# Optimization experiments

Measured on AMD Instinct MI355X. Metric: run time of the kernel, lower is better.

## Reference

```python
import jax, jax.numpy as jnp
import numpy as np

B, T, C = 2, 2048, 2048
H, KV, D = 16, 4, 128   # n_head, n_kv_head, head_dim
EPS = 1.1920929e-07     # torch.finfo(float32).eps, F.rms_norm default


def setup_inputs() -> dict:
    key = jax.random.key(0)
    ks = jax.random.split(key, 7)
    x = jax.random.normal(ks[0], (B, T, C), dtype=jnp.float32)
    # rope angles: cos/sin of positions, broadcastable to [B,T,H,D//2]
    inv_freq = 1.0 / (10000.0 ** (jnp.arange(0, D // 2, dtype=jnp.float32) / (D // 2)))
    ang = jnp.arange(T, dtype=jnp.float32)[:, None] * inv_freq[None, :]
    cos = jnp.cos(ang)[None, :, None, :]  # [1,T,1,D/2]
    sin = jnp.sin(ang)[None, :, None, :]
    s = 0.02
    Wq = jax.random.normal(ks[1], (C, H * D), dtype=jnp.float32) * s
    Wk = jax.random.normal(ks[2], (C, KV * D), dtype=jnp.float32) * s
    Wv = jax.random.normal(ks[3], (C, KV * D), dtype=jnp.float32) * s
    Wo = jax.random.normal(ks[4], (C, C), dtype=jnp.float32) * s
    return {"x": x, "cos": cos, "sin": sin, "Wq": Wq, "Wk": Wk, "Wv": Wv, "Wo": Wo}


def _rope(t, cos, sin):
    d = t.shape[-1] // 2
    t1, t2 = t[..., :d], t[..., d:]
    return jnp.concatenate([t1 * cos + t2 * sin, -t1 * sin + t2 * cos], axis=-1)


def _rmsnorm(t):
    return t * jax.lax.rsqrt(jnp.mean(t * t, axis=-1, keepdims=True) + EPS)


def reference(x, cos, sin, Wq, Wk, Wv, Wo):
    q = (x @ Wq).reshape(B, T, H, D)
    k = (x @ Wk).reshape(B, T, KV, D)
    v = (x @ Wv).reshape(B, T, KV, D)
    q = _rmsnorm(_rope(q, cos, sin))
    k = _rmsnorm(_rope(k, cos, sin))
    # [B, KV, G, T, D] query grouped per kv head (GQA)
    G = H // KV
    qh = q.transpose(0, 2, 1, 3).reshape(B, KV, G, T, D)
    kh = k.transpose(0, 2, 1, 3)  # [B, KV, T, D]
    vh = v.transpose(0, 2, 1, 3)
    scale = 1.0 / np.sqrt(D).astype(np.float32)
    scores = jnp.einsum('bhgqd,bhkd->bhgqk', qh, kh) * scale
    causal = jnp.tril(jnp.ones((T, T), dtype=bool))
    scores = jnp.where(causal, scores, jnp.finfo(scores.dtype).min)
    attn = jax.nn.softmax(scores, axis=-1)
    y = jnp.einsum('bhgqk,bhkd->bhgqd', attn, vh)  # [B,KV,G,T,D]
    y = y.reshape(B, H, T, D).transpose(0, 2, 1, 3).reshape(B, T, C)
    return y @ Wo
```

## Files before the change

### kernel.cpp

```cpp
#include <hip/hip_runtime.h>

using bf16x8 = __attribute__((ext_vector_type(8))) short;
using f32x4  = __attribute__((ext_vector_type(4))) float;

#define B_  2
#define T_  2048
#define C_  2048
#define H_  16
#define KV_ 4
#define D_  128

__device__ __forceinline__ unsigned short f2b(float f) {
  union { float f; unsigned int u; } v; v.f = f;
  unsigned int r = v.u + 0x7fffu + ((v.u >> 16) & 1u);
  return (unsigned short)(r >> 16);
}
__device__ __forceinline__ float b2f(unsigned short u) {
  union { unsigned int u; float f; } v; v.u = ((unsigned int)u) << 16;
  return v.f;
}
__device__ __forceinline__ unsigned int cvt_pk_bf16(float lo, float hi) {
  unsigned int r;
  asm("v_cvt_pk_bf16_f32 %0, %1, %2" : "=v"(r) : "v"(lo), "v"(hi));
  return r;
}
__device__ __forceinline__ void gld_lds16(const void* g, void* l) {
  __builtin_amdgcn_global_load_lds(
      (__attribute__((address_space(1))) void*)g,
      (__attribute__((address_space(3))) void*)l, 16, 0, 0);
}

__global__ void cast_bf16_k(const float* __restrict__ in, unsigned short* __restrict__ out) {
  int i = blockIdx.x * 256 + threadIdx.x;
  float4 f = ((const float4*)in)[i];
  ushort4 u; u.x = f2b(f.x); u.y = f2b(f.y); u.z = f2b(f.z); u.w = f2b(f.w);
  ((ushort4*)out)[i] = u;
}

__global__ void wtrans(const float* __restrict__ W, unsigned short* __restrict__ Wt,
                       int K, int N) {
  __shared__ float s[32][33];
  int n0 = blockIdx.x * 32, k0 = blockIdx.y * 32;
  int tx = threadIdx.x, ty = threadIdx.y;
  #pragma unroll
  for (int yy = 0; yy < 32; yy += 8)
    s[ty + yy][tx] = W[(size_t)(k0 + ty + yy) * N + n0 + tx];
  __syncthreads();
  #pragma unroll
  for (int yy = 0; yy < 32; yy += 8)
    Wt[(size_t)(n0 + ty + yy) * K + k0 + tx] = f2b(s[tx][ty + yy]);
}

template <bool OUT_BF16>
__device__ __forceinline__ void gemm_tile(
    const unsigned short* __restrict__ A, const unsigned short* __restrict__ Bt,
    void* __restrict__ Cv, int K, int ldc, int m0, int n0b, int n0c,
    unsigned short* sA, unsigned short* sB)
{
  const int tid  = threadIdx.x;
  const int lane = tid & 63, w = tid >> 6;
  const int quad = lane >> 4, l16 = lane & 15;
  const int wm = (w >> 1) * 64, wn = (w & 1) * 64;

  f32x4 acc[4][4] = {};

  const unsigned short* Abase = A  + (size_t)m0  * K;
  const unsigned short* Bbase = Bt + (size_t)n0b * K;

  for (int k0 = 0; k0 < K; k0 += 32) {
    #pragma unroll
    for (int r = 0; r < 2; ++r) {
      int c = tid + r * 256;
      int row = c >> 2, col = (c & 3) * 8;
      gld_lds16(Abase + (size_t)row * K + k0 + col, sA + c * 8);
      gld_lds16(Bbase + (size_t)row * K + k0 + col, sB + c * 8);
    }
    __syncthreads();
    bf16x8 af[4], bfr[4];
    #pragma unroll
    for (int i = 0; i < 4; ++i)
      af[i]  = *(const bf16x8*)(sA + (wm + i * 16 + l16) * 32 + quad * 8);
    #pragma unroll
    for (int j = 0; j < 4; ++j)
      bfr[j] = *(const bf16x8*)(sB + (wn + j * 16 + l16) * 32 + quad * 8);
    #pragma unroll
    for (int i = 0; i < 4; ++i)
      #pragma unroll
      for (int j = 0; j < 4; ++j)
        acc[i][j] = __builtin_amdgcn_mfma_f32_16x16x32_bf16(af[i], bfr[j], acc[i][j], 0, 0, 0);
    __syncthreads();
  }
  #pragma unroll
  for (int i = 0; i < 4; ++i) {
    #pragma unroll
    for (int r = 0; r < 4; ++r) {
      int row = m0 + wm + i * 16 + quad * 4 + r;
      #pragma unroll
      for (int j = 0; j < 4; ++j) {
        int col = n0c + wn + j * 16 + l16;
        float v = acc[i][j][r];
        if (OUT_BF16) ((unsigned short*)Cv)[(size_t)row * ldc + col] = f2b(v);
        else          ((float*)Cv)[(size_t)row * ldc + col] = v;
      }
    }
  }
}

__global__ void qkv_gemm(const unsigned short* __restrict__ xb,
                         const unsigned short* __restrict__ Wqt,
                         const unsigned short* __restrict__ Wkt,
                         const unsigned short* __restrict__ Wvt,
                         unsigned short* q, unsigned short* k, unsigned short* v) {
  __shared__ unsigned short sA[128 * 32], sB[128 * 32];
  int nt = blockIdx.x, mt = blockIdx.y;
  const unsigned short* Bt; unsigned short* C; int n0, ldc;
  if (nt < 16)      { Bt = Wqt; C = q; n0 = nt * 128;        ldc = H_ * D_;  }
  else if (nt < 20) { Bt = Wkt; C = k; n0 = (nt - 16) * 128; ldc = KV_ * D_; }
  else              { Bt = Wvt; C = v; n0 = (nt - 20) * 128; ldc = KV_ * D_; }
  gemm_tile<true>(xb, Bt, C, C_, ldc, mt * 128, n0, n0, sA, sB);
}

__global__ void out_gemm(const unsigned short* __restrict__ yb,
                         const unsigned short* __restrict__ Wot,
                         float* __restrict__ out) {
  __shared__ unsigned short sA[128 * 32], sB[128 * 32];
  gemm_tile<false>(yb, Wot, out, C_, C_, blockIdx.y * 128, blockIdx.x * 128, blockIdx.x * 128,
                   sA, sB);
}

template <int NH>
__global__ void ropenorm(const unsigned short* __restrict__ in,
                         const float* __restrict__ cs, const float* __restrict__ sn,
                         unsigned short* __restrict__ out, float oscale) {
  int row  = blockIdx.x * 4 + (threadIdx.x >> 6);
  int lane = threadIdx.x & 63;
  int head = row % NH;
  int t = (row / NH) & (T_ - 1);
  int b = row / (NH * T_);
  const unsigned short* p = in + (size_t)row * D_;
  float t1 = b2f(p[lane]), t2 = b2f(p[lane + 64]);
  float c = cs[t * 64 + lane], s = sn[t * 64 + lane];
  float o1 = t1 * c + t2 * s;
  float o2 = t2 * c - t1 * s;
  float ss = o1 * o1 + o2 * o2;
  #pragma unroll
  for (int off = 32; off > 0; off >>= 1) ss += __shfl_xor(ss, off, 64);
  float r = rsqrtf(ss * (1.0f / 128.0f) + 1.1920929e-07f) * oscale;
  size_t base = ((size_t)((b * NH + head) * 128 + (t >> 4))) * 2048 + (size_t)(t & 15) * 8;
  out[base + (size_t)(lane >> 3) * 128 + (lane & 7)]       = f2b(o1 * r);
  out[base + (size_t)(8 + (lane >> 3)) * 128 + (lane & 7)] = f2b(o2 * r);
}

__global__ void vfrag_k(const unsigned short* __restrict__ v, unsigned short* __restrict__ vf) {
  int it = blockIdx.x;
  int b = blockIdx.y >> 2, kv = blockIdx.y & 3;
  int d = threadIdx.x, ty = threadIdx.y;
  int t0 = it * 64;
  size_t obase = ((size_t)((b * KV_ + kv) * 32 + it)) * 8192
               + (size_t)(d >> 4) * 1024 + (size_t)(d & 15) * 8;
  #pragma unroll
  for (int tcg = 0; tcg < 4; ++tcg) {
    int tc = ty * 4 + tcg;
    unsigned short val[8];
    #pragma unroll
    for (int e = 0; e < 8; ++e)
      val[e] = v[(((size_t)(b * T_) + t0 + tc * 8 + e) * KV_ + kv) * D_ + d];
    ushort4 u0 = {val[0], val[1], val[2], val[3]};
    ushort4 u1 = {val[4], val[5], val[6], val[7]};
    *(ushort4*)(vf + obase + (size_t)tc * 128)     = u0;
    *(ushort4*)(vf + obase + (size_t)tc * 128 + 4) = u1;
  }
}

__global__ __launch_bounds__(256, 2) void attn_kernel(
    const unsigned short* __restrict__ qf, const unsigned short* __restrict__ kf,
    const unsigned short* __restrict__ vf, unsigned short* __restrict__ yb) {
  __shared__ __align__(16) char smem[34048];

  const int xp = (int)blockIdx.x;
  const int b = xp >> 2, kv = xp & 3;
  const int yp = (int)blockIdx.y;
  const int j = yp >> 2, hp = yp & 3;
  const int tid = threadIdx.x;
  const int w = tid >> 6, lane = tid & 63;
  const int quad = lane >> 4, l16 = lane & 15;
  const int qsel = w & 1, half = w >> 1;
  const int qt = qsel ? (63 - j) : j;
  const int h = kv * 4 + hp;
  const int q0 = qt * 32;
  const int ntile = (qt >> 1) + 1;
  unsigned short* myP = (unsigned short*)smem + w * (32 * 72);

  const unsigned short* Qf = qf + ((size_t)(b * H_ + h) * 128 + qt * 2) * 2048;
  const unsigned short* Kf = kf + (size_t)(b * KV_ + kv) * 128 * 2048;
  const unsigned short* Vf = vf + (size_t)(b * KV_ + kv) * 32 * 8192;

  bf16x8 bq[2][4];
  #pragma unroll
  for (int i = 0; i < 2; ++i)
    #pragma unroll
    for (int kk = 0; kk < 4; ++kk)
      bq[i][kk] = *(const bf16x8*)(Qf + (size_t)i * 2048 + (kk * 4 + quad) * 128 + l16 * 8);

  float l_i[2] = {0.f, 0.f};
  f32x4 o[2][8] = {};

  for (int it = half; it < ntile; it += 2) {
    const int t0 = it * 64;
    const unsigned short* Kt = Kf + (size_t)(it * 4) * 2048;
    const unsigned short* Vt = Vf + (size_t)it * 8192;

    f32x4 sc[4][2] = {};
    #pragma unroll
    for (int kk = 0; kk < 4; ++kk) {
      bf16x8 ak[4];
      #pragma unroll
      for (int jt = 0; jt < 4; ++jt)
        ak[jt] = *(const bf16x8*)(Kt + (size_t)jt * 2048 + (kk * 4 + quad) * 128 + l16 * 8);
      #pragma unroll
      for (int jt = 0; jt < 4; ++jt)
        #pragma unroll
        for (int i = 0; i < 2; ++i)
          sc[jt][i] = __builtin_amdgcn_mfma_f32_16x16x32_bf16(ak[jt], bq[i][kk], sc[jt][i], 0, 0, 0);
    }

    bf16x8 bv[2][8];
    #pragma unroll
    for (int kk2 = 0; kk2 < 2; ++kk2)
      #pragma unroll
      for (int jj = 0; jj < 8; ++jj)
        bv[kk2][jj] = *(const bf16x8*)(Vt + (size_t)jj * 1024 + (kk2 * 4 + quad) * 128 + l16 * 8);

    if (it == ntile - 1) {
      #pragma unroll
      for (int jt = 0; jt < 4; ++jt) {
        int kg = t0 + jt * 16 + quad * 4;
        #pragma unroll
        for (int i = 0; i < 2; ++i) {
          int qg = q0 + i * 16 + l16;
          #pragma unroll
          for (int r = 0; r < 4; ++r)
            if (kg + r > qg) sc[jt][i][r] = -3.0e38f;
        }
      }
    }

    #pragma unroll
    for (int i = 0; i < 2; ++i) {
      float part = 0.f;
      #pragma unroll
      for (int jt = 0; jt < 4; ++jt)
        #pragma unroll
        for (int r = 0; r < 4; ++r) {
          float p = __expf(sc[jt][i][r] - 12.0f);
          sc[jt][i][r] = p; part += p;
        }
      l_i[i] += part;
    }

    #pragma unroll
    for (int i = 0; i < 2; ++i)
      #pragma unroll
      for (int jt = 0; jt < 4; ++jt) {
        uint2 uu;
        uu.x = cvt_pk_bf16(sc[jt][i][0], sc[jt][i][1]);
        uu.y = cvt_pk_bf16(sc[jt][i][2], sc[jt][i][3]);
        *(uint2*)(myP + (i * 16 + l16) * 72 + jt * 16 + quad * 4) = uu;
      }

    #pragma unroll
    for (int kk2 = 0; kk2 < 2; ++kk2) {
      bf16x8 ap[2];
      #pragma unroll
      for (int i = 0; i < 2; ++i)
        ap[i] = *(const bf16x8*)(myP + (i * 16 + l16) * 72 + kk2 * 32 + quad * 8);
      #pragma unroll
      for (int i = 0; i < 2; ++i)
        #pragma unroll
        for (int jj = 0; jj < 8; ++jj)
          o[i][jj] = __builtin_amdgcn_mfma_f32_16x16x32_bf16(ap[i], bv[kk2][jj], o[i][jj], 0, 0, 0);
    }
  }

  float lsum[2];
  #pragma unroll
  for (int i = 0; i < 2; ++i) {
    float l = l_i[i];
    l += __shfl_xor(l, 16, 64);
    l += __shfl_xor(l, 32, 64);
    lsum[i] = l;
  }

  __syncthreads();
  float* oc = (float*)smem + qsel * (32 * 132);
  float* lc = (float*)smem + 2 * (32 * 132) + qsel * 32;
  if (half == 1) {
    #pragma unroll
    for (int i = 0; i < 2; ++i) {
      if (quad == 0) lc[i * 16 + l16] = lsum[i];
      #pragma unroll
      for (int jj = 0; jj < 8; ++jj)
        #pragma unroll
        for (int r = 0; r < 4; ++r)
          oc[(i * 16 + quad * 4 + r) * 132 + jj * 16 + l16] = o[i][jj][r];
    }
  }
  __syncthreads();
  if (half == 0) {
    #pragma unroll
    for (int i = 0; i < 2; ++i) {
      float l = lsum[i] + lc[i * 16 + l16];
      float linv = 1.0f / l;
      float lr[4];
      #pragma unroll
      for (int r = 0; r < 4; ++r) lr[r] = __shfl(linv, quad * 4 + r, 64);
      #pragma unroll
      for (int r = 0; r < 4; ++r) {
        int tg = q0 + i * 16 + quad * 4 + r;
        unsigned short* yr = yb + (((size_t)(b * T_ + tg)) * H_ + h) * D_;
        #pragma unroll
        for (int jj = 0; jj < 8; ++jj) {
          float vsum = o[i][jj][r] + oc[(i * 16 + quad * 4 + r) * 132 + jj * 16 + l16];
          yr[jj * 16 + l16] = f2b(vsum * lr[r]);
        }
      }
    }
  }
}

extern "C" void kernel_launch(void* const* d_in, const int* in_sizes, int n_in,
                              void* d_out, int out_size, void* d_ws, size_t ws_size,
                              hipStream_t stream) {
  (void)in_sizes; (void)n_in; (void)out_size; (void)ws_size;
  const float* x  = (const float*)d_in[0];
  const float* cs = (const float*)d_in[1];
  const float* sn = (const float*)d_in[2];
  const float* Wq = (const float*)d_in[3];
  const float* Wk = (const float*)d_in[4];
  const float* Wv = (const float*)d_in[5];
  const float* Wo = (const float*)d_in[6];
  float* out = (float*)d_out;
  char* ws = (char*)d_ws;

  unsigned short* xb   = (unsigned short*)(ws + 0);
  unsigned short* Wqt  = (unsigned short*)(ws + 16777216);
  unsigned short* Wkt  = (unsigned short*)(ws + 25165824);
  unsigned short* Wvt  = (unsigned short*)(ws + 27262976);
  unsigned short* Wot  = (unsigned short*)(ws + 29360128);
  unsigned short* qraw = (unsigned short*)(ws + 37748736);
  unsigned short* kraw = (unsigned short*)(ws + 54525952);
  unsigned short* vraw = (unsigned short*)(ws + 58720256);
  unsigned short* qfr  = (unsigned short*)(ws + 62914560);
  unsigned short* kfr  = (unsigned short*)(ws + 79691776);
  unsigned short* vfr  = (unsigned short*)(ws + 83886080);
  unsigned short* yb   = qraw;

  cast_bf16_k<<<dim3(8192), dim3(256), 0, stream>>>(x, xb);
  wtrans<<<dim3(64, 64), dim3(32, 8), 0, stream>>>(Wq, Wqt, 2048, 2048);
  wtrans<<<dim3(16, 64), dim3(32, 8), 0, stream>>>(Wk, Wkt, 2048, 512);
  wtrans<<<dim3(16, 64), dim3(32, 8), 0, stream>>>(Wv, Wvt, 2048, 512);
  wtrans<<<dim3(64, 64), dim3(32, 8), 0, stream>>>(Wo, Wot, 2048, 2048);
  qkv_gemm<<<dim3(24, 32), dim3(256), 0, stream>>>(xb, Wqt, Wkt, Wvt, qraw, kraw, vraw);
  ropenorm<16><<<dim3(16384), dim3(256), 0, stream>>>(qraw, cs, sn, qfr, 0.08838834764831845f);
  ropenorm<4><<<dim3(4096),  dim3(256), 0, stream>>>(kraw, cs, sn, kfr, 1.0f);
  vfrag_k<<<dim3(32, 8), dim3(128, 2), 0, stream>>>(vraw, vfr);
  attn_kernel<<<dim3(8, 128), dim3(256), 0, stream>>>(qfr, kfr, vfr, yb);
  out_gemm<<<dim3(16, 32), dim3(256), 0, stream>>>(yb, Wot, out);
}
```

Before: 318.5 us.

## Replace QKV GEMM with 256x256 tile, 8-wave, double-buffered direct-to-LDS kernel

Replaces the 128x128 QKV projection GEMM with a 256x256-tile kernel using 512 threads, async global-to-LDS loads into double-buffered swizzled LDS, and interleaved MFMA/load phases with priority hints. Blocks are remapped so each XCD handles adjacent M rows, which improves L2 reuse of the x tile. The goal is higher arithmetic intensity and overlap of memory loads with MFMA work. In exchange, 192 blocks on 256 CUs leaves some CUs idle, and the large LDS and register footprint reduces occupancy.

```diff
diff --git a/kernel.cpp b/kernel.cpp
--- a/kernel.cpp
+++ b/kernel.cpp
@@ -106,26 +106,149 @@
   }
 }
 
-__global__ void qkv_gemm(const unsigned short* __restrict__ xb,
-                         const unsigned short* __restrict__ Wqt,
-                         const unsigned short* __restrict__ Wkt,
-                         const unsigned short* __restrict__ Wvt,
-                         unsigned short* q, unsigned short* k, unsigned short* v) {
-  __shared__ unsigned short sA[128 * 32], sB[128 * 32];
-  int nt = blockIdx.x, mt = blockIdx.y;
-  const unsigned short* Bt; unsigned short* C; int n0, ldc;
-  if (nt < 16)      { Bt = Wqt; C = q; n0 = nt * 128;        ldc = H_ * D_;  }
-  else if (nt < 20) { Bt = Wkt; C = k; n0 = (nt - 16) * 128; ldc = KV_ * D_; }
-  else              { Bt = Wvt; C = v; n0 = (nt - 20) * 128; ldc = KV_ * D_; }
-  gemm_tile<true>(xb, Bt, C, C_, ldc, mt * 128, n0, n0, sA, sB);
-}
-
 __global__ void out_gemm(const unsigned short* __restrict__ yb,
                          const unsigned short* __restrict__ Wot,
                          float* __restrict__ out) {
   __shared__ unsigned short sA[128 * 32], sB[128 * 32];
   gemm_tile<false>(yb, Wot, out, C_, C_, blockIdx.y * 128, blockIdx.x * 128, blockIdx.x * 128,
                    sA, sB);
+}
+
+__global__ __launch_bounds__(512, 2) void qkv_gemm8(
+    const unsigned short* __restrict__ xb,
+    const unsigned short* __restrict__ Wqt,
+    const unsigned short* __restrict__ Wkt,
+    const unsigned short* __restrict__ Wvt,
+    unsigned short* __restrict__ q, unsigned short* __restrict__ k,
+    unsigned short* __restrict__ v) {
+  __shared__ unsigned short lds[65536];
+
+  const int id  = (int)blockIdx.x;
+  const int xcd = id & 7, jj = id >> 3;
+  const int mt  = xcd * 2 + jj / 12;
+  const int nt  = jj % 12;
+
+  const unsigned short* Bt; unsigned short* Cp; int n0, ldc;
+  if (nt < 8)       { Bt = Wqt; Cp = q; n0 = nt * 256;        ldc = 2048; }
+  else if (nt < 10) { Bt = Wkt; Cp = k; n0 = (nt - 8) * 256;  ldc = 512;  }
+  else              { Bt = Wvt; Cp = v; n0 = (nt - 10) * 256; ldc = 512;  }
+  const int m0 = mt * 256;
+
+  const int tid = (int)threadIdx.x;
+  const int w = tid >> 6, lane = tid & 63;
+  const int quad = lane >> 4, l16 = lane & 15;
+  const int wr = w >> 2, wc = w & 3;
+  const int swz = (l16 & 12) << 1;
+
+  const unsigned short* Ab = xb + (size_t)m0 * 2048;
+  const unsigned short* Bb = Bt + (size_t)n0 * 2048;
+
+  const int c0 = tid, c1 = tid + 512;
+  const int r0 = c0 >> 2, r1 = c1 >> 2;
+  const int x0 = ((c0 & 3) * 8) ^ (((c0 >> 4) & 3) << 3);
+  const int x1 = ((c1 & 3) * 8) ^ (((c1 >> 4) & 3) << 3);
+
+#define STAGE_A(buf, kh, kb) do { \
+    unsigned short* d_ = lds + (buf) * 16384 + (kh) * 8192; \
+    gld_lds16(Ab + (size_t)r0 * 2048 + (kb) + (kh) * 32 + x0, d_ + c0 * 8); \
+    gld_lds16(Ab + (size_t)r1 * 2048 + (kb) + (kh) * 32 + x1, d_ + c1 * 8); \
+  } while (0)
+#define STAGE_B(buf, kh, kb) do { \
+    unsigned short* d_ = lds + 32768 + (buf) * 16384 + (kh) * 8192; \
+    gld_lds16(Bb + (size_t)r0 * 2048 + (kb) + (kh) * 32 + x0, d_ + c0 * 8); \
+    gld_lds16(Bb + (size_t)r1 * 2048 + (kb) + (kh) * 32 + x1, d_ + c1 * 8); \
+  } while (0)
+
+  f32x4 acc[8][4] = {};
+
+  STAGE_A(0, 0, 0); STAGE_B(0, 0, 0); STAGE_A(0, 1, 0); STAGE_B(0, 1, 0);
+  asm volatile("s_waitcnt vmcnt(4)" ::: "memory");
+  __builtin_amdgcn_s_barrier();
+
+  const unsigned short* aLd = lds + (wr * 128 + l16) * 32 + (quad * 8 ^ swz);
+  const unsigned short* bLd = lds + 32768 + (wc * 64 + l16) * 32 + (quad * 8 ^ swz);
+
+  for (int t = 0; t < 32; ++t) {
+    const int cur = t & 1, nxt = cur ^ 1;
+    const bool more = (t < 31);
+    const int kb = (t + 1) * 64;
+    const int off = cur * 16384;
+    bf16x8 a[8], bbr[4];
+
+    #pragma unroll
+    for (int m = 0; m < 8; ++m) a[m] = *(const bf16x8*)(aLd + off + m * 512);
+    #pragma unroll
+    for (int n = 0; n < 4; ++n) bbr[n] = *(const bf16x8*)(bLd + off + n * 512);
+    if (more) STAGE_A(nxt, 0, kb);
+    __builtin_amdgcn_s_barrier();
+    asm volatile("s_waitcnt lgkmcnt(0)" ::: "memory");
+    __builtin_amdgcn_sched_barrier(0);
+    __builtin_amdgcn_s_setprio(1);
+    #pragma unroll
+    for (int m = 0; m < 4; ++m)
+      #pragma unroll
+      for (int n = 0; n < 4; ++n)
+        acc[m][n] = __builtin_amdgcn_mfma_f32_16x16x32_bf16(a[m], bbr[n], acc[m][n], 0, 0, 0);
+    __builtin_amdgcn_s_setprio(0);
+    __builtin_amdgcn_s_barrier();
+
+    if (more) STAGE_B(nxt, 0, kb);
+    __builtin_amdgcn_s_barrier();
+    __builtin_amdgcn_s_setprio(1);
+    #pragma unroll
+    for (int m = 4; m < 8; ++m)
+      #pragma unroll
+      for (int n = 0; n < 4; ++n)
+        acc[m][n] = __builtin_amdgcn_mfma_f32_16x16x32_bf16(a[m], bbr[n], acc[m][n], 0, 0, 0);
+    __builtin_amdgcn_s_setprio(0);
+    if (more) asm volatile("s_waitcnt vmcnt(4)" ::: "memory");
+    else      asm volatile("s_waitcnt vmcnt(0)" ::: "memory");
+    __builtin_amdgcn_s_barrier();
+
+    #pragma unroll
+    for (int m = 0; m < 8; ++m) a[m] = *(const bf16x8*)(aLd + off + 8192 + m * 512);
+    #pragma unroll
+    for (int n = 0; n < 4; ++n) bbr[n] = *(const bf16x8*)(bLd + off + 8192 + n * 512);
+    if (more) STAGE_A(nxt, 1, kb);
+    __builtin_amdgcn_s_barrier();
+    asm volatile("s_waitcnt lgkmcnt(0)" ::: "memory");
+    __builtin_amdgcn_sched_barrier(0);
+    __builtin_amdgcn_s_setprio(1);
+    #pragma unroll
+    for (int m = 0; m < 4; ++m)
+      #pragma unroll
+      for (int n = 0; n < 4; ++n)
+        acc[m][n] = __builtin_amdgcn_mfma_f32_16x16x32_bf16(a[m], bbr[n], acc[m][n], 0, 0, 0);
+    __builtin_amdgcn_s_setprio(0);
+    __builtin_amdgcn_s_barrier();
+
+    if (more) STAGE_B(nxt, 1, kb);
+    __builtin_amdgcn_s_barrier();
+    __builtin_amdgcn_s_setprio(1);
+    #pragma unroll
+    for (int m = 4; m < 8; ++m)
+      #pragma unroll
+      for (int n = 0; n < 4; ++n)
+        acc[m][n] = __builtin_amdgcn_mfma_f32_16x16x32_bf16(a[m], bbr[n], acc[m][n], 0, 0, 0);
+    __builtin_amdgcn_s_setprio(0);
+    if (more) asm volatile("s_waitcnt vmcnt(4)" ::: "memory");
+    else      asm volatile("s_waitcnt vmcnt(0)" ::: "memory");
+    __builtin_amdgcn_s_barrier();
+  }
+#undef STAGE_A
+#undef STAGE_B
+
+  #pragma unroll
+  for (int m = 0; m < 8; ++m)
+    #pragma unroll
+    for (int r = 0; r < 4; ++r) {
+      int row = m0 + wr * 128 + m * 16 + quad * 4 + r;
+      #pragma unroll
+      for (int n = 0; n < 4; ++n) {
+        int col = n0 + wc * 64 + n * 16 + l16;
+        Cp[(size_t)row * ldc + col] = f2b(acc[m][n][r]);
+      }
+    }
 }
 
 template <int NH>
@@ -360,7 +483,7 @@
   wtrans<<<dim3(16, 64), dim3(32, 8), 0, stream>>>(Wk, Wkt, 2048, 512);
   wtrans<<<dim3(16, 64), dim3(32, 8), 0, stream>>>(Wv, Wvt, 2048, 512);
   wtrans<<<dim3(64, 64), dim3(32, 8), 0, stream>>>(Wo, Wot, 2048, 2048);
-  qkv_gemm<<<dim3(24, 32), dim3(256), 0, stream>>>(xb, Wqt, Wkt, Wvt, qraw, kraw, vraw);
+  qkv_gemm8<<<dim3(192), dim3(512), 0, stream>>>(xb, Wqt, Wkt, Wvt, qraw, kraw, vraw);
   ropenorm<16><<<dim3(16384), dim3(256), 0, stream>>>(qraw, cs, sn, qfr, 0.08838834764831845f);
   ropenorm<4><<<dim3(4096),  dim3(256), 0, stream>>>(kraw, cs, sn, kfr, 1.0f);
   vfrag_k<<<dim3(32, 8), dim3(128, 2), 0, stream>>>(vraw, vfr);
```

Result: no change. 323.5 us (+1.6%).
